# Optimization experiments

Hardware: AMD Instinct MI355X
Metric: run time of the kernel (lower is better)

## Reference

```python
import jax, jax.numpy as jnp
import numpy as np

B, S, D, H, DFF, L, V = 2, 512, 768, 12, 3072, 12, 32000
DK = D // H
LN_EPS = 1e-5


def setup_inputs() -> dict:
    key = jax.random.key(0)
    ks = jax.random.split(key, 24)
    s = 0.02
    n = lambda k, shp: (s * jax.random.normal(k, shp)).astype(jnp.float32)
    return dict(
        tokens=jax.random.randint(ks[0], (B, S), 0, V, dtype=jnp.int32),
        tok_emb=n(ks[1], (V, D)),
        pos_emb=n(ks[2], (S, D)),
        ln1_s=jnp.ones((L, D), jnp.float32), ln1_b=jnp.zeros((L, D), jnp.float32),
        Wq=n(ks[3], (L, D, D)), bq=jnp.zeros((L, D), jnp.float32),
        Wk=n(ks[4], (L, D, D)), bk=jnp.zeros((L, D), jnp.float32),
        Wv=n(ks[5], (L, D, D)), bv=jnp.zeros((L, D), jnp.float32),
        Wo=n(ks[6], (L, D, D)), bo=jnp.zeros((L, D), jnp.float32),
        ln2_s=jnp.ones((L, D), jnp.float32), ln2_b=jnp.zeros((L, D), jnp.float32),
        W1=n(ks[7], (L, D, DFF)), b1=jnp.zeros((L, DFF), jnp.float32),
        W2=n(ks[8], (L, DFF, D)), b2=jnp.zeros((L, D), jnp.float32),
        W_out=n(ks[9], (D, V)), b_out=jnp.zeros((V,), jnp.float32),
    )


def _layernorm(x, scale, bias):
    mu = jnp.mean(x, axis=-1, keepdims=True)
    var = jnp.mean(jnp.square(x - mu), axis=-1, keepdims=True)
    return (x - mu) * jax.lax.rsqrt(var + LN_EPS) * scale + bias


def _gpt1_forward(tokens, tok_emb, pos_emb, ln1_s, ln1_b, Wq, bq, Wk, bk, Wv, bv,
                  Wo, bo, ln2_s, ln2_b, W1, b1, W2, b2, W_out, b_out):
    b, s = tokens.shape
    x = tok_emb[tokens] + pos_emb[:s][None]  # [B,S,D]

    def step(x, p):
        (l1s, l1b, wq, bq_, wk, bk_, wv, bv_, wo, bo_, l2s, l2b, w1, b1_, w2, b2_) = p
        x2 = _layernorm(x, l1s, l1b)
        q = (x2 @ wq + bq_).reshape(b, s, H, DK)
        k = (x2 @ wk + bk_).reshape(b, s, H, DK)
        v = (x2 @ wv + bv_).reshape(b, s, H, DK)
        # NOTE: source has no causal mask (full bidirectional attention).
        scores = jnp.einsum('bqhd,bkhd->bhqk', q, k) / jnp.sqrt(jnp.float32(DK))
        attn = jax.nn.softmax(scores, axis=-1)
        ctx = jnp.einsum('bhqk,bkhd->bqhd', attn, v).reshape(b, s, D)
        x = x + ctx @ wo + bo_
        x2 = _layernorm(x, l2s, l2b)
        # torch nn.GELU default = exact (erf) GELU
        h = jax.nn.gelu(x2 @ w1 + b1_, approximate=False)
        x = x + h @ w2 + b2_
        return x, None

    params = (ln1_s, ln1_b, Wq, bq, Wk, bk, Wv, bv, Wo, bo,
              ln2_s, ln2_b, W1, b1, W2, b2)
    x, _ = jax.lax.scan(step, x, params)
    return x @ W_out + b_out  # [B,S,V]


def reference(tokens, tok_emb, pos_emb, ln1_s, ln1_b, Wq, bq, Wk, bk, Wv, bv,
              Wo, bo, ln2_s, ln2_b, W1, b1, W2, b2, W_out, b_out):
    return _gpt1_forward(tokens, tok_emb, pos_emb, ln1_s, ln1_b, Wq, bq, Wk, bk,
                         Wv, bv, Wo, bo, ln2_s, ln2_b, W1, b1, W2, b2, W_out, b_out)
```

## Files before the change

### kernel.cpp

```cpp
#include <hip/hip_runtime.h>
#include <hip/hip_bf16.h>
#include <math.h>

constexpr int BATCH = 2;
constexpr int SEQ   = 512;
constexpr int DM    = 768;
constexpr int NH    = 12;
constexpr int FF    = 3072;
constexpr int NL    = 12;
constexpr int NV    = 32000;
constexpr int HD    = 64;
constexpr int MT    = BATCH * SEQ;
constexpr int QKV   = 3 * DM;

typedef __attribute__((ext_vector_type(8))) short bf16x8;
typedef __attribute__((ext_vector_type(4))) float f32x4;

__device__ __forceinline__ float b2f(ushort u) {
    return __uint_as_float(((unsigned)u) << 16);
}
__device__ __forceinline__ ushort f2b(float f) {
    __hip_bfloat16 h = __float2bfloat16(f);
    return *reinterpret_cast<ushort*>(&h);
}

template<int N>
__device__ __forceinline__ void waitcnt_vm() {
    if constexpr (N == 0) asm volatile("s_waitcnt vmcnt(0)" ::: "memory");
    else if constexpr (N == 2) asm volatile("s_waitcnt vmcnt(2)" ::: "memory");
    else if constexpr (N == 3) asm volatile("s_waitcnt vmcnt(3)" ::: "memory");
    else if constexpr (N == 4) asm volatile("s_waitcnt vmcnt(4)" ::: "memory");
    else if constexpr (N == 6) asm volatile("s_waitcnt vmcnt(6)" ::: "memory");
    else if constexpr (N == 8) asm volatile("s_waitcnt vmcnt(8)" ::: "memory");
}

__global__ void embed_kernel(const int* __restrict__ tokens,
                             const float* __restrict__ tok_emb,
                             const float* __restrict__ pos_emb,
                             float* __restrict__ x) {
    int m = blockIdx.x;
    int s = m % SEQ;
    int t = tokens[m];
    const float* te = tok_emb + (size_t)t * DM;
    const float* pe = pos_emb + (size_t)s * DM;
    float* row = x + (size_t)m * DM;
    for (int d = threadIdx.x; d < DM; d += blockDim.x)
        row[d] = te[d] + pe[d];
}

__global__ __launch_bounds__(256) void wconv_kernel(
        const float* __restrict__ W, ushort* __restrict__ out,
        int K, int N, size_t inLS, size_t outLS, int nOff) {
    int l  = blockIdx.z;
    int n0 = blockIdx.x * 64;
    int k0 = blockIdx.y * 64;
    int tid = threadIdx.x;
    __shared__ float t[64][65];
    const float* src = W + (size_t)l * inLS + (size_t)k0 * N + n0;
    int r  = tid >> 4;
    int c4 = (tid & 15) * 4;
#pragma unroll
    for (int i = 0; i < 4; i++) {
        int row = i * 16 + r;
        float4 v = *(const float4*)(src + (size_t)row * N + c4);
        t[row][c4 + 0] = v.x; t[row][c4 + 1] = v.y;
        t[row][c4 + 2] = v.z; t[row][c4 + 3] = v.w;
    }
    __syncthreads();
    ushort* dst = out + (size_t)l * outLS;
#pragma unroll
    for (int i = 0; i < 4; i++) {
        int rr = i * 16 + r;
        ushort4 o;
        o.x = f2b(t[c4 + 0][rr]); o.y = f2b(t[c4 + 1][rr]);
        o.z = f2b(t[c4 + 2][rr]); o.w = f2b(t[c4 + 3][rr]);
        *(ushort4*)(dst + (size_t)(nOff + n0 + rr) * K + k0 + c4) = o;
    }
}

__global__ void biaspack_kernel(const float* __restrict__ bq,
                                const float* __restrict__ bk,
                                const float* __restrict__ bv,
                                float* __restrict__ bqkv) {
    int idx = blockIdx.x * 256 + threadIdx.x;
    if (idx >= NL * QKV) return;
    int l = idx / QKV, c = idx % QKV;
    float v;
    if (c < DM)            v = bq[l * DM + c];
    else if (c < 2 * DM)   v = bk[l * DM + c - DM];
    else                   v = bv[l * DM + c - 2 * DM];
    bqkv[idx] = v;
}

__global__ void cvt_kernel(const float* __restrict__ in, ushort* __restrict__ out, int n) {
    int i = blockIdx.x * 256 + threadIdx.x;
    if (i < n) out[i] = f2b(in[i]);
}

__global__ __launch_bounds__(256) void ln_kernel(const float* __restrict__ x,
                                                 const float* __restrict__ sc,
                                                 const float* __restrict__ bi,
                                                 ushort* __restrict__ y) {
    int m = blockIdx.x;
    int t = threadIdx.x;
    const float* row = x + (size_t)m * DM;
    float vals[3];
    float s0 = 0.f, s1 = 0.f;
#pragma unroll
    for (int i = 0; i < 3; i++) {
        float v = row[t + 256 * i];
        vals[i] = v;
        s0 += v;
        s1 += v * v;
    }
#pragma unroll
    for (int off = 32; off >= 1; off >>= 1) {
        s0 += __shfl_down(s0, off, 64);
        s1 += __shfl_down(s1, off, 64);
    }
    __shared__ float r0[4], r1[4];
    __shared__ float mu_s, rs_s;
    int wid = t >> 6, lane = t & 63;
    if (lane == 0) { r0[wid] = s0; r1[wid] = s1; }
    __syncthreads();
    if (t == 0) {
        float a = r0[0] + r0[1] + r0[2] + r0[3];
        float q = r1[0] + r1[1] + r1[2] + r1[3];
        float mu  = a / DM;
        float var = q / DM - mu * mu;
        mu_s = mu;
        rs_s = rsqrtf(var + 1e-5f);
    }
    __syncthreads();
    float mu = mu_s, rs = rs_s;
    ushort* orow = y + (size_t)m * DM;
#pragma unroll
    for (int i = 0; i < 3; i++) {
        int d = t + 256 * i;
        orow[d] = f2b((vals[i] - mu) * rs * sc[d] + bi[d]);
    }
}

__device__ __forceinline__ void gload_lds16(const void* g, void* l) {
    __builtin_amdgcn_global_load_lds(
        (const __attribute__((address_space(1))) void*)g,
        (__attribute__((address_space(3))) void*)l, 16, 0, 0);
}

template<int BM, int BN, int WM, int WN, int NBUF, int SPLITK, int ACT,
         bool RES, bool WF32, bool WBF16, bool VT, bool ATOMIC>
__global__ __launch_bounds__(WM * WN * 64) void mfma_gemm(
        const ushort* __restrict__ A, const ushort* __restrict__ BT,
        const float* __restrict__ bias, const float* __restrict__ res,
        float* __restrict__ Cf, ushort* __restrict__ Cb, ushort* __restrict__ Vt,
        int M, int N, int K) {
    constexpr int THREADS = WM * WN * 64;
    constexpr int ROWS    = BM + BN;
    constexpr int RND     = ROWS * 4 / THREADS;
    constexpr int MR      = BM / WM / 16;
    constexpr int NR      = BN / WN / 16;
    constexpr int STRIDE  = ROWS * 32;
    __shared__ ushort S_lds[NBUF * STRIDE];
    int tid = threadIdx.x;
    int il = tid & 63, wv = tid >> 6;

    int p   = blockIdx.x + gridDim.x * blockIdx.y;
    int nwg = gridDim.x * gridDim.y;
    int q8  = nwg >> 3, r8 = nwg & 7;
    int xcd = p & 7, k8 = p >> 3;
    int orig = (xcd < r8 ? xcd * (q8 + 1) : r8 * (q8 + 1) + (xcd - r8) * q8) + k8;
    int bx = orig / gridDim.y;
    int by = orig % gridDim.y;
    int bm = by * BM, bn = bx * BN;

    int kLen  = K / SPLITK;
    int kBase = blockIdx.z * kLen;

    const ushort* src[RND];
    int dstOff[RND];
#pragma unroll
    for (int r = 0; r < RND; r++) {
        int f = r * THREADS + tid;
        int row = f >> 2, seg = f & 3;
        int lseg = seg ^ ((row >> 1) & 3);
        src[r] = (row < BM ? A + (size_t)(bm + row) * K
                           : BT + (size_t)(bn + row - BM) * K) + kBase + lseg * 8;
        dstOff[r] = (r * THREADS + wv * 64) * 8;
    }

    int wm = wv / WN, wn = wv % WN;
    int lr = il & 15;
    int lkS = ((il >> 4) ^ ((lr >> 1) & 3)) * 8;
    f32x4 acc[MR][NR] = {};

    int nt = kLen >> 5;

#pragma unroll
    for (int b = 0; b < NBUF - 1; b++)
#pragma unroll
        for (int r = 0; r < RND; r++)
            gload_lds16(src[r] + b * 32, &S_lds[b * STRIDE + dstOff[r]]);
    waitcnt_vm<RND * (NBUF - 2)>();
    __builtin_amdgcn_s_barrier();

    int cur = 0;
    for (int t = 0; t < nt; ++t) {
        if (t + NBUF - 1 < nt) {
            int sb = cur + NBUF - 1; if (sb >= NBUF) sb -= NBUF;
            int kofs = (t + NBUF - 1) * 32;
            ushort* Bp = &S_lds[sb * STRIDE];
#pragma unroll
            for (int r = 0; r < RND; r++) gload_lds16(src[r] + kofs, &Bp[dstOff[r]]);
        }

        const ushort* base = &S_lds[cur * STRIDE];
        bf16x8 af[MR], bfr[NR];
#pragma unroll
        for (int i = 0; i < MR; i++)
            af[i] = *(const bf16x8*)&base[(wm * (BM / WM) + i * 16 + lr) * 32 + lkS];
#pragma unroll
        for (int i = 0; i < NR; i++)
            bfr[i] = *(const bf16x8*)&base[(BM + wn * (BN / WN) + i * 16 + lr) * 32 + lkS];
        __builtin_amdgcn_s_setprio(1);
#pragma unroll
        for (int mi = 0; mi < MR; mi++)
#pragma unroll
            for (int ni = 0; ni < NR; ni++)
                acc[mi][ni] = __builtin_amdgcn_mfma_f32_16x16x32_bf16(
                    af[mi], bfr[ni], acc[mi][ni], 0, 0, 0);
        __builtin_amdgcn_s_setprio(0);

        if (t + 1 < nt) {
            int k = nt - t - 2;
            if (k > NBUF - 2) k = NBUF - 2;
            switch (k) {
                case 0:  waitcnt_vm<0>(); break;
                case 1:  waitcnt_vm<RND>(); break;
                default: waitcnt_vm<2 * RND>(); break;
            }
            __builtin_amdgcn_s_barrier();
        }
        cur = (cur + 1 == NBUF) ? 0 : cur + 1;
    }

    bool addBias = bias && (SPLITK == 1 || blockIdx.z == 0);
#pragma unroll
    for (int mi = 0; mi < MR; mi++) {
        int row0 = bm + wm * (BM / WM) + mi * 16 + (il >> 4) * 4;
#pragma unroll
        for (int ni = 0; ni < NR; ni++) {
            int col = bn + wn * (BN / WN) + ni * 16 + (il & 15);
            float bv = addBias ? bias[col] : 0.f;
#pragma unroll
            for (int j = 0; j < 4; j++) {
                int r = row0 + j;
                float v = acc[mi][ni][j] + bv;
                if (ACT == 1) v = 0.5f * v * (1.0f + erff(v * 0.70710678118654752f));
                if (RES) v += res[(size_t)r * N + col];
                if (ATOMIC) atomicAdd(&Cf[(size_t)r * N + col], v);
                else if (WF32) Cf[(size_t)r * N + col] = v;
                if (WBF16) {
                    if (VT && bn >= 2 * DM) {
                        int d  = col - 2 * DM;
                        int hh = d >> 6, dd = d & 63;
                        int bb = r >> 9, s = r & (SEQ - 1);
                        Vt[((size_t)(bb * NH + hh) * HD + dd) * SEQ + s] = f2b(v);
                    } else {
                        Cb[(size_t)r * N + col] = f2b(v);
                    }
                }
            }
        }
    }
}

__device__ __forceinline__ char* swzp(void* base, int row, int colByte) {
    return (char*)base + ((row * 128 + colByte) ^ ((row & 7) << 4));
}
__device__ __forceinline__ const char* swzpc(const void* base, int row, int colByte) {
    return (const char*)base + ((row * 128 + colByte) ^ ((row & 7) << 4));
}

__global__ __launch_bounds__(256) void fattn_kernel(
        const ushort* __restrict__ qkv, const ushort* __restrict__ vt,
        ushort* __restrict__ ctx) {
    int qt = blockIdx.x;
    int h  = blockIdx.y;
    int b  = blockIdx.z;
    int tid = threadIdx.x;
    int il = tid & 63, wv = tid >> 6;
    int qsub = wv & 1, grp = wv >> 1;

    __shared__ __align__(16) char smem[41 * 1024];
    ushort* Ks = (ushort*)(smem + grp * 8192);
    ushort* Vs = (ushort*)(smem + 16384 + grp * 8192);
    ushort* Ps = (ushort*)(smem + 32768 + wv * 2048);
    float*  Om = (float*)smem;
    float*  Ss = (float*)(smem + 16384);

    int bh = b * NH + h;
    const ushort* kbase = qkv + (size_t)b * SEQ * QKV + DM + h * HD;
    const ushort* vbase = vt + (size_t)bh * HD * SEQ;

    int lr = il & 15, lg = il >> 4;
    int qrow = qt * 32 + qsub * 16 + lr;
    const ushort* qptr = qkv + (size_t)(b * SEQ + qrow) * QKV + h * HD + lg * 8;
    bf16x8 qf0 = *(const bf16x8*)qptr;
    bf16x8 qf1 = *(const bf16x8*)(qptr + 32);

    f32x4 accO[4] = {};
    float sm[4] = {0.f, 0.f, 0.f, 0.f};

    int lig  = qsub * 64 + il;
    int srow = lig >> 3;
    int sseg = (lig & 7) * 8;

    for (int kt = 0; kt < 4; kt++) {
        int k0 = grp * 256 + kt * 64;
        bf16x8 kreg[4], vreg[4];
#pragma unroll
        for (int r = 0; r < 4; r++) {
            int row = r * 16 + srow;
            kreg[r] = *(const bf16x8*)(kbase + (size_t)(k0 + row) * QKV + sseg);
            vreg[r] = *(const bf16x8*)(vbase + (size_t)row * SEQ + k0 + sseg);
        }
        __syncthreads();
#pragma unroll
        for (int r = 0; r < 4; r++) {
            int row = r * 16 + srow;
            *(bf16x8*)swzp(Ks, row, sseg * 2) = kreg[r];
            *(bf16x8*)swzp(Vs, row, sseg * 2) = vreg[r];
        }
        __syncthreads();

        f32x4 accS[4] = {};
        __builtin_amdgcn_s_setprio(1);
#pragma unroll
        for (int nf = 0; nf < 4; nf++) {
            bf16x8 b0 = *(const bf16x8*)swzpc(Ks, nf * 16 + lr, lg * 16);
            bf16x8 b1 = *(const bf16x8*)swzpc(Ks, nf * 16 + lr, 64 + lg * 16);
            accS[nf] = __builtin_amdgcn_mfma_f32_16x16x32_bf16(qf0, b0, accS[nf], 0, 0, 0);
            accS[nf] = __builtin_amdgcn_mfma_f32_16x16x32_bf16(qf1, b1, accS[nf], 0, 0, 0);
        }
        __builtin_amdgcn_s_setprio(0);

        float pv[4][4];
#pragma unroll
        for (int nf = 0; nf < 4; nf++)
#pragma unroll
            for (int j = 0; j < 4; j++)
                pv[nf][j] = __expf(fmaf(accS[nf][j], 0.125f, -8.0f));
#pragma unroll
        for (int j = 0; j < 4; j++) {
            float rs = (pv[0][j] + pv[1][j]) + (pv[2][j] + pv[3][j]);
            rs += __shfl_xor(rs, 1, 64);
            rs += __shfl_xor(rs, 2, 64);
            rs += __shfl_xor(rs, 4, 64);
            rs += __shfl_xor(rs, 8, 64);
            sm[j] += rs;
        }

#pragma unroll
        for (int nf = 0; nf < 4; nf++)
#pragma unroll
            for (int j = 0; j < 4; j++)
                *(ushort*)swzp(Ps, lg * 4 + j, (nf * 16 + lr) * 2) = f2b(pv[nf][j]);

        bf16x8 pa0 = *(const bf16x8*)swzpc(Ps, lr, lg * 16);
        bf16x8 pa1 = *(const bf16x8*)swzpc(Ps, lr, 64 + lg * 16);
        __builtin_amdgcn_s_setprio(1);
#pragma unroll
        for (int nf = 0; nf < 4; nf++) {
            bf16x8 v0 = *(const bf16x8*)swzpc(Vs, nf * 16 + lr, lg * 16);
            bf16x8 v1 = *(const bf16x8*)swzpc(Vs, nf * 16 + lr, 64 + lg * 16);
            accO[nf] = __builtin_amdgcn_mfma_f32_16x16x32_bf16(pa0, v0, accO[nf], 0, 0, 0);
            accO[nf] = __builtin_amdgcn_mfma_f32_16x16x32_bf16(pa1, v1, accO[nf], 0, 0, 0);
        }
        __builtin_amdgcn_s_setprio(0);
    }

    __syncthreads();
    if (grp == 1) {
#pragma unroll
        for (int nf = 0; nf < 4; nf++)
#pragma unroll
            for (int j = 0; j < 4; j++)
                Om[(qsub * 16 + lg * 4 + j) * 64 + nf * 16 + lr] = accO[nf][j];
        if (lr == 0) {
#pragma unroll
            for (int j = 0; j < 4; j++)
                Ss[qsub * 16 + lg * 4 + j] = sm[j];
        }
    }
    __syncthreads();
    if (grp == 0) {
        ushort* obase = ctx + (size_t)(b * SEQ + qt * 32 + qsub * 16) * DM + h * HD;
#pragma unroll
        for (int j = 0; j < 4; j++) {
            int q = lg * 4 + j;
            float inv = 1.0f / (sm[j] + Ss[qsub * 16 + q]);
#pragma unroll
            for (int nf = 0; nf < 4; nf++) {
                int d = nf * 16 + lr;
                float o1 = Om[(qsub * 16 + q) * 64 + d];
                obase[(size_t)q * DM + d] = f2b((accO[nf][j] + o1) * inv);
            }
        }
    }
}

extern "C" void kernel_launch(void* const* d_in, const int* in_sizes, int n_in,
                              void* d_out, int out_size, void* d_ws, size_t ws_size,
                              hipStream_t stream) {
    const int*   tokens  = (const int*)d_in[0];
    const float* tok_emb = (const float*)d_in[1];
    const float* pos_emb = (const float*)d_in[2];
    const float* ln1_s   = (const float*)d_in[3];
    const float* ln1_b   = (const float*)d_in[4];
    const float* Wq      = (const float*)d_in[5];
    const float* bq      = (const float*)d_in[6];
    const float* Wk      = (const float*)d_in[7];
    const float* bk      = (const float*)d_in[8];
    const float* Wv      = (const float*)d_in[9];
    const float* bv      = (const float*)d_in[10];
    const float* Wo      = (const float*)d_in[11];
    const float* bo      = (const float*)d_in[12];
    const float* ln2_s   = (const float*)d_in[13];
    const float* ln2_b   = (const float*)d_in[14];
    const float* W1      = (const float*)d_in[15];
    const float* b1      = (const float*)d_in[16];
    const float* W2      = (const float*)d_in[17];
    const float* b2      = (const float*)d_in[18];
    const float* W_out   = (const float*)d_in[19];
    const float* b_out   = (const float*)d_in[20];

    char* ws = (char*)d_ws;
    size_t off = 0;
    auto alloc = [&](size_t bytes) { size_t o = off; off = (off + bytes + 255) & ~(size_t)255; return o; };

    float*  x    = (float*)(ws + alloc((size_t)MT * DM * 4));
    ushort* x2b  = (ushort*)(ws + alloc((size_t)MT * DM * 2));
    ushort* qkvb = (ushort*)(ws + alloc((size_t)MT * QKV * 2));
    ushort* cb   = (ushort*)(ws + alloc((size_t)MT * DM * 2));
    ushort* hb   = (ushort*)(ws + alloc((size_t)MT * FF * 2));
    ushort* xb   = (ushort*)(ws + alloc((size_t)MT * DM * 2));
    ushort* vtb  = (ushort*)(ws + alloc((size_t)BATCH * NH * HD * SEQ * 2));
    float*  bqkv = (float*)(ws + alloc((size_t)NL * QKV * 4));

    size_t szQkvT = (size_t)NL * QKV * DM;
    size_t szWoT  = (size_t)NL * DM * DM;
    size_t szW1T  = (size_t)NL * FF * DM;
    size_t szW2T  = (size_t)NL * DM * FF;
    size_t szWoutT= (size_t)NV * DM;

    size_t actEnd = off;
    size_t fullNeed = actEnd + 2 * (szQkvT + szWoT + szW1T + szW2T + szWoutT) + 5 * 256;
    bool full = (fullNeed <= ws_size);

    ushort *WqkvT, *WoT, *W1T, *W2T, *WoutT;
    if (full) {
        WqkvT = (ushort*)(ws + alloc(szQkvT * 2));
        WoT   = (ushort*)(ws + alloc(szWoT * 2));
        W1T   = (ushort*)(ws + alloc(szW1T * 2));
        W2T   = (ushort*)(ws + alloc(szW2T * 2));
        WoutT = (ushort*)(ws + alloc(szWoutT * 2));
    } else {
        size_t layerElems = (size_t)QKV * DM + (size_t)DM * DM + 2 * (size_t)FF * DM;
        size_t regionElems = layerElems > szWoutT ? layerElems : szWoutT;
        ushort* region = (ushort*)(ws + alloc(regionElems * 2));
        WqkvT = region;
        WoT   = WqkvT + (size_t)QKV * DM;
        W1T   = WoT + (size_t)DM * DM;
        W2T   = W1T + (size_t)FF * DM;
        WoutT = region;
    }

    biaspack_kernel<<<(NL * QKV + 255) / 256, 256, 0, stream>>>(bq, bk, bv, bqkv);
    embed_kernel<<<MT, 256, 0, stream>>>(tokens, tok_emb, pos_emb, x);

    if (full) {
        dim3 gD(DM / 64, DM / 64, NL);
        wconv_kernel<<<gD, 256, 0, stream>>>(Wq, WqkvT, DM, DM, (size_t)DM * DM, (size_t)QKV * DM, 0);
        wconv_kernel<<<gD, 256, 0, stream>>>(Wk, WqkvT, DM, DM, (size_t)DM * DM, (size_t)QKV * DM, DM);
        wconv_kernel<<<gD, 256, 0, stream>>>(Wv, WqkvT, DM, DM, (size_t)DM * DM, (size_t)QKV * DM, 2 * DM);
        wconv_kernel<<<gD, 256, 0, stream>>>(Wo, WoT, DM, DM, (size_t)DM * DM, (size_t)DM * DM, 0);
        dim3 g1(FF / 64, DM / 64, NL);
        wconv_kernel<<<g1, 256, 0, stream>>>(W1, W1T, DM, FF, (size_t)DM * FF, (size_t)FF * DM, 0);
        dim3 g2(DM / 64, FF / 64, NL);
        wconv_kernel<<<g2, 256, 0, stream>>>(W2, W2T, FF, DM, (size_t)FF * DM, (size_t)DM * FF, 0);
        dim3 go(NV / 64, DM / 64, 1);
        wconv_kernel<<<go, 256, 0, stream>>>(W_out, WoutT, DM, NV, 0, 0, 0);
    }

    for (int l = 0; l < NL; l++) {
        ushort* wqkv = WqkvT + (full ? (size_t)l * QKV * DM : 0);
        ushort* wo   = WoT   + (full ? (size_t)l * DM * DM  : 0);
        ushort* w1   = W1T   + (full ? (size_t)l * FF * DM  : 0);
        ushort* w2   = W2T   + (full ? (size_t)l * DM * FF  : 0);
        if (!full) {
            dim3 gD(DM / 64, DM / 64, 1);
            wconv_kernel<<<gD, 256, 0, stream>>>(Wq + (size_t)l * DM * DM, wqkv, DM, DM, 0, 0, 0);
            wconv_kernel<<<gD, 256, 0, stream>>>(Wk + (size_t)l * DM * DM, wqkv, DM, DM, 0, 0, DM);
            wconv_kernel<<<gD, 256, 0, stream>>>(Wv + (size_t)l * DM * DM, wqkv, DM, DM, 0, 0, 2 * DM);
            wconv_kernel<<<gD, 256, 0, stream>>>(Wo + (size_t)l * DM * DM, wo, DM, DM, 0, 0, 0);
            dim3 g1(FF / 64, DM / 64, 1);
            wconv_kernel<<<g1, 256, 0, stream>>>(W1 + (size_t)l * DM * FF, w1, DM, FF, 0, 0, 0);
            dim3 g2(DM / 64, FF / 64, 1);
            wconv_kernel<<<g2, 256, 0, stream>>>(W2 + (size_t)l * FF * DM, w2, FF, DM, 0, 0, 0);
        }

        ln_kernel<<<MT, 256, 0, stream>>>(x, ln1_s + l * DM, ln1_b + l * DM, x2b);

        mfma_gemm<64, 128, 2, 2, 4, 1, 0, false, false, true, true, false>
            <<<dim3(QKV / 128, MT / 64), 256, 0, stream>>>(
            x2b, wqkv, bqkv + (size_t)l * QKV, nullptr, nullptr, qkvb, vtb, MT, QKV, DM);

        fattn_kernel<<<dim3(SEQ / 32, NH, BATCH), 256, 0, stream>>>(qkvb, vtb, cb);

        mfma_gemm<64, 64, 2, 2, 4, 2, 0, false, false, false, false, true>
            <<<dim3(DM / 64, MT / 64, 2), 256, 0, stream>>>(
            cb, wo, bo + (size_t)l * DM, nullptr, x, nullptr, nullptr, MT, DM, DM);

        ln_kernel<<<MT, 256, 0, stream>>>(x, ln2_s + l * DM, ln2_b + l * DM, x2b);

        mfma_gemm<64, 128, 2, 2, 4, 1, 1, false, false, true, false, false>
            <<<dim3(FF / 128, MT / 64), 256, 0, stream>>>(
            x2b, w1, b1 + (size_t)l * FF, nullptr, nullptr, hb, nullptr, MT, FF, DM);

        mfma_gemm<64, 64, 2, 2, 4, 4, 0, false, false, false, false, true>
            <<<dim3(DM / 64, MT / 64, 4), 256, 0, stream>>>(
            hb, w2, b2 + (size_t)l * DM, nullptr, x, nullptr, nullptr, MT, DM, FF);
    }

    if (!full) {
        dim3 go(NV / 64, DM / 64, 1);
        wconv_kernel<<<go, 256, 0, stream>>>(W_out, WoutT, DM, NV, 0, 0, 0);
    }
    cvt_kernel<<<(MT * DM + 255) / 256, 256, 0, stream>>>(x, xb, MT * DM);

    mfma_gemm<256, 256, 2, 4, 3, 1, 0, false, true, false, false, false>
        <<<dim3(NV / 256, MT / 256), 512, 0, stream>>>(
        xb, WoutT, b_out, nullptr, (float*)d_out, nullptr, nullptr, MT, NV, DM);
}
```

Before: 1.267 ms.

## Widen weight-transpose tiles, wrap GEMM instances as named kernels, retune split-K and buffers

The weight conversion kernel now handles 128 K-rows per block and writes 16-byte contiguous bf16 runs per thread, which cuts the grid in half and widens stores. The templated GEMM becomes a device body wrapped by named kernels. The W2 GEMM drops from split-K 4 to 2, and the logits GEMM moves from 3 to 4 LDS buffers. Fewer atomics and a deeper pipeline are traded against less parallelism and more shared memory.

```diff
diff --git a/kernel.cpp b/kernel.cpp
--- a/kernel.cpp
+++ b/kernel.cpp
@@ -53,28 +53,32 @@
         int K, int N, size_t inLS, size_t outLS, int nOff) {
     int l  = blockIdx.z;
     int n0 = blockIdx.x * 64;
-    int k0 = blockIdx.y * 64;
+    int k0 = blockIdx.y * 128;
     int tid = threadIdx.x;
-    __shared__ float t[64][65];
+    __shared__ float t[2][64][65];
     const float* src = W + (size_t)l * inLS + (size_t)k0 * N + n0;
     int r  = tid >> 4;
     int c4 = (tid & 15) * 4;
 #pragma unroll
-    for (int i = 0; i < 4; i++) {
-        int row = i * 16 + r;
-        float4 v = *(const float4*)(src + (size_t)row * N + c4);
-        t[row][c4 + 0] = v.x; t[row][c4 + 1] = v.y;
-        t[row][c4 + 2] = v.z; t[row][c4 + 3] = v.w;
+    for (int i = 0; i < 8; i++) {
+        int krow = i * 16 + r;
+        float4 v = *(const float4*)(src + (size_t)krow * N + c4);
+        float* dstl = &t[krow >> 6][krow & 63][c4];
+        dstl[0] = v.x; dstl[1] = v.y; dstl[2] = v.z; dstl[3] = v.w;
     }
     __syncthreads();
     ushort* dst = out + (size_t)l * outLS;
-#pragma unroll
-    for (int i = 0; i < 4; i++) {
-        int rr = i * 16 + r;
-        ushort4 o;
-        o.x = f2b(t[c4 + 0][rr]); o.y = f2b(t[c4 + 1][rr]);
-        o.z = f2b(t[c4 + 2][rr]); o.w = f2b(t[c4 + 3][rr]);
-        *(ushort4*)(dst + (size_t)(nOff + n0 + rr) * K + k0 + c4) = o;
+    int kk = (tid & 15) * 8;
+    int h  = kk >> 6;
+    int kb = kk & 63;
+#pragma unroll
+    for (int j = 0; j < 4; j++) {
+        int n = j * 16 + (tid >> 4);
+        ushort o[8];
+#pragma unroll
+        for (int m = 0; m < 8; m++) o[m] = f2b(t[h][kb + m][n]);
+        *(ushort4*)(dst + (size_t)(nOff + n0 + n) * K + k0 + kk)     = *(ushort4*)&o[0];
+        *(ushort4*)(dst + (size_t)(nOff + n0 + n) * K + k0 + kk + 4) = *(ushort4*)&o[4];
     }
 }
 
@@ -149,7 +153,7 @@
 
 template<int BM, int BN, int WM, int WN, int NBUF, int SPLITK, int ACT,
          bool RES, bool WF32, bool WBF16, bool VT, bool ATOMIC>
-__global__ __launch_bounds__(WM * WN * 64) void mfma_gemm(
+__device__ __forceinline__ void gemm_body(
         const ushort* __restrict__ A, const ushort* __restrict__ BT,
         const float* __restrict__ bias, const float* __restrict__ res,
         float* __restrict__ Cf, ushort* __restrict__ Cb, ushort* __restrict__ Vt,
@@ -272,6 +276,37 @@
             }
         }
     }
+}
+
+__global__ __launch_bounds__(256) void gemm_qkv(
+        const ushort* A, const ushort* BT, const float* bias,
+        ushort* Cb, ushort* Vt, int M, int N, int K) {
+    gemm_body<64, 128, 2, 2, 4, 1, 0, false, false, true, true, false>(
+        A, BT, bias, nullptr, nullptr, Cb, Vt, M, N, K);
+}
+__global__ __launch_bounds__(256) void gemm_wo(
+        const ushort* A, const ushort* BT, const float* bias,
+        float* Cf, int M, int N, int K) {
+    gemm_body<64, 64, 2, 2, 4, 2, 0, false, false, false, false, true>(
+        A, BT, bias, nullptr, Cf, nullptr, nullptr, M, N, K);
+}
+__global__ __launch_bounds__(256) void gemm_w1(
+        const ushort* A, const ushort* BT, const float* bias,
+        ushort* Cb, int M, int N, int K) {
+    gemm_body<64, 128, 2, 2, 4, 1, 1, false, false, true, false, false>(
+        A, BT, bias, nullptr, nullptr, Cb, nullptr, M, N, K);
+}
+__global__ __launch_bounds__(256) void gemm_w2(
+        const ushort* A, const ushort* BT, const float* bias,
+        float* Cf, int M, int N, int K) {
+    gemm_body<64, 64, 2, 2, 4, 2, 0, false, false, false, false, true>(
+        A, BT, bias, nullptr, Cf, nullptr, nullptr, M, N, K);
+}
+__global__ __launch_bounds__(512) void gemm_logits(
+        const ushort* A, const ushort* BT, const float* bias,
+        float* Cf, int M, int N, int K) {
+    gemm_body<256, 256, 2, 4, 4, 1, 0, false, true, false, false, false>(
+        A, BT, bias, nullptr, Cf, nullptr, nullptr, M, N, K);
 }
 
 __device__ __forceinline__ char* swzp(void* base, int row, int colByte) {
@@ -479,16 +514,16 @@
     embed_kernel<<<MT, 256, 0, stream>>>(tokens, tok_emb, pos_emb, x);
 
     if (full) {
-        dim3 gD(DM / 64, DM / 64, NL);
+        dim3 gD(DM / 64, DM / 128, NL);
         wconv_kernel<<<gD, 256, 0, stream>>>(Wq, WqkvT, DM, DM, (size_t)DM * DM, (size_t)QKV * DM, 0);
         wconv_kernel<<<gD, 256, 0, stream>>>(Wk, WqkvT, DM, DM, (size_t)DM * DM, (size_t)QKV * DM, DM);
         wconv_kernel<<<gD, 256, 0, stream>>>(Wv, WqkvT, DM, DM, (size_t)DM * DM, (size_t)QKV * DM, 2 * DM);
         wconv_kernel<<<gD, 256, 0, stream>>>(Wo, WoT, DM, DM, (size_t)DM * DM, (size_t)DM * DM, 0);
-        dim3 g1(FF / 64, DM / 64, NL);
+        dim3 g1(FF / 64, DM / 128, NL);
         wconv_kernel<<<g1, 256, 0, stream>>>(W1, W1T, DM, FF, (size_t)DM * FF, (size_t)FF * DM, 0);
-        dim3 g2(DM / 64, FF / 64, NL);
+        dim3 g2(DM / 64, FF / 128, NL);
         wconv_kernel<<<g2, 256, 0, stream>>>(W2, W2T, FF, DM, (size_t)FF * DM, (size_t)DM * FF, 0);
-        dim3 go(NV / 64, DM / 64, 1);
+        dim3 go(NV / 64, DM / 128, 1);
         wconv_kernel<<<go, 256, 0, stream>>>(W_out, WoutT, DM, NV, 0, 0, 0);
     }
 
@@ -498,47 +533,42 @@
         ushort* w1   = W1T   + (full ? (size_t)l * FF * DM  : 0);
         ushort* w2   = W2T   + (full ? (size_t)l * DM * FF  : 0);
         if (!full) {
-            dim3 gD(DM / 64, DM / 64, 1);
+            dim3 gD(DM / 64, DM / 128, 1);
             wconv_kernel<<<gD, 256, 0, stream>>>(Wq + (size_t)l * DM * DM, wqkv, DM, DM, 0, 0, 0);
             wconv_kernel<<<gD, 256, 0, stream>>>(Wk + (size_t)l * DM * DM, wqkv, DM, DM, 0, 0, DM);
             wconv_kernel<<<gD, 256, 0, stream>>>(Wv + (size_t)l * DM * DM, wqkv, DM, DM, 0, 0, 2 * DM);
             wconv_kernel<<<gD, 256, 0, stream>>>(Wo + (size_t)l * DM * DM, wo, DM, DM, 0, 0, 0);
-            dim3 g1(FF / 64, DM / 64, 1);
+            dim3 g1(FF / 64, DM / 128, 1);
             wconv_kernel<<<g1, 256, 0, stream>>>(W1 + (size_t)l * DM * FF, w1, DM, FF, 0, 0, 0);
-            dim3 g2(DM / 64, FF / 64, 1);
+            dim3 g2(DM / 64, FF / 128, 1);
             wconv_kernel<<<g2, 256, 0, stream>>>(W2 + (size_t)l * FF * DM, w2, FF, DM, 0, 0, 0);
         }
 
         ln_kernel<<<MT, 256, 0, stream>>>(x, ln1_s + l * DM, ln1_b + l * DM, x2b);
 
-        mfma_gemm<64, 128, 2, 2, 4, 1, 0, false, false, true, true, false>
-            <<<dim3(QKV / 128, MT / 64), 256, 0, stream>>>(
-            x2b, wqkv, bqkv + (size_t)l * QKV, nullptr, nullptr, qkvb, vtb, MT, QKV, DM);
+        gemm_qkv<<<dim3(QKV / 128, MT / 64), 256, 0, stream>>>(
+            x2b, wqkv, bqkv + (size_t)l * QKV, qkvb, vtb, MT, QKV, DM);
 
         fattn_kernel<<<dim3(SEQ / 32, NH, BATCH), 256, 0, stream>>>(qkvb, vtb, cb);
 
-        mfma_gemm<64, 64, 2, 2, 4, 2, 0, false, false, false, false, true>
-            <<<dim3(DM / 64, MT / 64, 2), 256, 0, stream>>>(
-            cb, wo, bo + (size_t)l * DM, nullptr, x, nullptr, nullptr, MT, DM, DM);
+        gemm_wo<<<dim3(DM / 64, MT / 64, 2), 256, 0, stream>>>(
+            cb, wo, bo + (size_t)l * DM, x, MT, DM, DM);
 
         ln_kernel<<<MT, 256, 0, stream>>>(x, ln2_s + l * DM, ln2_b + l * DM, x2b);
 
-        mfma_gemm<64, 128, 2, 2, 4, 1, 1, false, false, true, false, false>
-            <<<dim3(FF / 128, MT / 64), 256, 0, stream>>>(
-            x2b, w1, b1 + (size_t)l * FF, nullptr, nullptr, hb, nullptr, MT, FF, DM);
-
-        mfma_gemm<64, 64, 2, 2, 4, 4, 0, false, false, false, false, true>
-            <<<dim3(DM / 64, MT / 64, 4), 256, 0, stream>>>(
-            hb, w2, b2 + (size_t)l * DM, nullptr, x, nullptr, nullptr, MT, DM, FF);
+        gemm_w1<<<dim3(FF / 128, MT / 64), 256, 0, stream>>>(
+            x2b, w1, b1 + (size_t)l * FF, hb, MT, FF, DM);
+
+        gemm_w2<<<dim3(DM / 64, MT / 64, 2), 256, 0, stream>>>(
+            hb, w2, b2 + (size_t)l * DM, x, MT, DM, FF);
     }
 
     if (!full) {
-        dim3 go(NV / 64, DM / 64, 1);
+        dim3 go(NV / 64, DM / 128, 1);
         wconv_kernel<<<go, 256, 0, stream>>>(W_out, WoutT, DM, NV, 0, 0, 0);
     }
     cvt_kernel<<<(MT * DM + 255) / 256, 256, 0, stream>>>(x, xb, MT * DM);
 
-    mfma_gemm<256, 256, 2, 4, 3, 1, 0, false, true, false, false, false>
-        <<<dim3(NV / 256, MT / 256), 512, 0, stream>>>(
-        xb, WoutT, b_out, nullptr, (float*)d_out, nullptr, nullptr, MT, NV, DM);
-}
+    gemm_logits<<<dim3(NV / 256, MT / 256), 512, 0, stream>>>(
+        xb, WoutT, b_out, (float*)d_out, MT, NV, DM);
+}
```

Result: no change. 1.271 ms (+0.3%).
